# Kernel optimization log

Measured on AMD Instinct MI355X. Metric: run time of the kernel, lower is better.

## Reference

```python
import jax, jax.numpy as jnp
import numpy as np
from math import pi as PI

N_NODES = 50000
N_EDGES = 1000000
HIDDEN = 128
N_GAUSS = 50
N_FILT = 128
N_COLORS = 4
CUTOFF = 10.0
LOG2 = float(np.log(2.0))


def setup_inputs() -> dict:
    key = jax.random.key(0)
    ks = jax.random.split(key, 16)
    glorot = jax.nn.initializers.glorot_uniform()
    inp = {
        "x": jax.random.normal(ks[0], (N_NODES, HIDDEN), jnp.float32),
        "edge_index": jax.random.randint(ks[1], (2, N_EDGES), 0, N_NODES),
        "edge_weight": jax.random.uniform(ks[2], (N_EDGES,), jnp.float32) * CUTOFF,
        "edge_attr": jax.random.normal(ks[3], (N_EDGES, N_GAUSS), jnp.float32),
        "colors": jax.random.randint(ks[4], (N_EDGES,), 0, N_COLORS),
        # ColoredMLP params, stacked over colors
        "mlp1_w": glorot(ks[5], (N_COLORS, N_FILT, N_GAUSS), jnp.float32),
        "mlp1_b": jnp.zeros((N_COLORS, N_FILT), jnp.float32),
        "mlp2_w": glorot(ks[6], (N_COLORS, N_FILT, N_FILT), jnp.float32),
        "mlp2_b": jnp.zeros((N_COLORS, N_FILT), jnp.float32),
        # CFConv linears
        "lin1_w": glorot(ks[7], (N_FILT, HIDDEN), jnp.float32),
        "lin2_w": glorot(ks[8], (HIDDEN, N_FILT), jnp.float32),
        "lin2_b": jnp.zeros((HIDDEN,), jnp.float32),
        # final Linear
        "lin_w": glorot(ks[9], (HIDDEN, HIDDEN), jnp.float32),
        "lin_b": jnp.zeros((HIDDEN,), jnp.float32),
    }
    return inp


def shifted_softplus(v):
    return jax.nn.softplus(v) - LOG2


def colored_mlp(edge_attr, colors, mlp1_w, mlp1_b, mlp2_w, mlp2_b):
    # per-color small MLP; loop over the small fixed color set, select by mask
    out = jnp.zeros((edge_attr.shape[0], N_FILT), edge_attr.dtype)
    for c in range(N_COLORS):
        h = shifted_softplus(edge_attr @ mlp1_w[c].T + mlp1_b[c])
        h = h @ mlp2_w[c].T + mlp2_b[c]
        out = jnp.where((colors == c)[:, None], h, out)
    return out


def reference(x, edge_index, edge_weight, edge_attr, colors,
              mlp1_w, mlp1_b, mlp2_w, mlp2_b,
              lin1_w, lin2_w, lin2_b, lin_w, lin_b):
    # cosine cutoff
    C = 0.5 * (jnp.cos(edge_weight * PI / CUTOFF) + 1.0)  # [E]
    W = colored_mlp(edge_attr, colors, mlp1_w, mlp1_b, mlp2_w, mlp2_b) * C[:, None]  # [E,F]
    h = x @ lin1_w.T  # [N,F]
    src, dst = edge_index[0], edge_index[1]
    msg = h[src] * W  # gather + modulate, [E,F]
    agg = jax.ops.segment_sum(msg, dst, num_segments=N_NODES)  # scatter-add, [N,F]
    out = agg @ lin2_w.T + lin2_b  # [N,H]
    out = shifted_softplus(out)
    out = out @ lin_w.T + lin_b
    return out
```

## Files before the change

### kernel.cpp

```cpp
#include <hip/hip_runtime.h>
#include <math.h>

#define N_NODES_ 50000
#define N_EDGES_ 1000000
#define HID 128
#define NG 50
#define NF 128
#define NCOL 4
#define CSEG 258048
#define NKEY (NCOL * N_NODES_)
#define CHUNK 625
#define NCHUNK_PER_C 80
#define NCHUNK (NCOL * NCHUNK_PER_C)

typedef short s16x8 __attribute__((ext_vector_type(8)));
typedef float f32x4 __attribute__((ext_vector_type(4)));

__device__ __forceinline__ float sspf(float v) {
    float r = __logf(1.f + __expf(v)) - 0.69314718055994531f;
    return (v > 15.f) ? (v - 0.69314718055994531f) : r;
}

__device__ __forceinline__ unsigned int f2b(float f) {
    unsigned int u = __float_as_uint(f);
    return (u + 0x7fffu + ((u >> 16) & 1u)) >> 16;
}

__global__ __launch_bounds__(256) void hist_kernel(const int* __restrict__ colors,
                                                   const int* __restrict__ edge_index,
                                                   int* __restrict__ hist) {
    int e = blockIdx.x * 256 + threadIdx.x;
    if (e < N_EDGES_) {
        int key = colors[e] * N_NODES_ + edge_index[N_EDGES_ + e];
        atomicAdd(&hist[key], 1);
    }
}

__global__ __launch_bounds__(256) void scan1_kernel(int* __restrict__ hist,
                                                    int* __restrict__ csum) {
    __shared__ int s[CHUNK];
    int b = blockIdx.x;
    int c = b / NCHUNK_PER_C, ch = b % NCHUNK_PER_C;
    int gofs = c * N_NODES_ + ch * CHUNK;
    for (int i = threadIdx.x; i < CHUNK; i += 256) s[i] = hist[gofs + i];
    __syncthreads();
    if (threadIdx.x == 0) {
        int run = 0;
        for (int i = 0; i < CHUNK; ++i) { int t = s[i]; s[i] = run; run += t; }
        csum[b] = run;
    }
    __syncthreads();
    for (int i = threadIdx.x; i < CHUNK; i += 256) hist[gofs + i] = s[i];
}

__global__ __launch_bounds__(64) void scan2_kernel(const int* __restrict__ csum,
                                                   int* __restrict__ cbase,
                                                   int* __restrict__ g_cnt) {
    int c = threadIdx.x;
    if (c < NCOL) {
        int run = 0;
        for (int j = 0; j < NCHUNK_PER_C; ++j) {
            cbase[c * NCHUNK_PER_C + j] = run;
            run += csum[c * NCHUNK_PER_C + j];
        }
        g_cnt[c] = run;
    }
}

__global__ __launch_bounds__(256) void scan3_kernel(int* __restrict__ hist,
                                                    const int* __restrict__ cbase) {
    int b = blockIdx.x;
    int c = b / NCHUNK_PER_C, ch = b % NCHUNK_PER_C;
    int gofs = c * N_NODES_ + ch * CHUNK;
    int add = cbase[b];
    for (int i = threadIdx.x; i < CHUNK; i += 256) hist[gofs + i] += add;
}

__global__ __launch_bounds__(256) void scatter_kernel(const int* __restrict__ colors,
                                                      const int* __restrict__ edge_index,
                                                      int* __restrict__ base,
                                                      int* __restrict__ eid_s) {
    int e = blockIdx.x * 256 + threadIdx.x;
    if (e < N_EDGES_) {
        int c = colors[e];
        int key = c * N_NODES_ + edge_index[N_EDGES_ + e];
        int r = atomicAdd(&base[key], 1);
        eid_s[c * CSEG + r] = e;
    }
}

__global__ __launch_bounds__(256) void wconv_kernel(const float* __restrict__ m1w,
                                                    const float* __restrict__ m2w,
                                                    unsigned short* __restrict__ m1b16,
                                                    unsigned short* __restrict__ m2b16) {
    int idx = blockIdx.x * 256 + threadIdx.x;
    if (idx < NCOL * NF * 64) {
        int c = idx / (NF * 64);
        int rem = idx % (NF * 64);
        int n = rem / 64, k = rem % 64;
        float v = (k < NG) ? m1w[(c * NF + n) * NG + k] : 0.f;
        m1b16[idx] = (unsigned short)f2b(v);
    } else if (idx < NCOL * NF * 64 + NCOL * NF * NF) {
        int j = idx - NCOL * NF * 64;
        m2b16[j] = (unsigned short)f2b(m2w[j]);
    }
}

__global__ __launch_bounds__(256, 4) void passA_kernel(
    const int* __restrict__ edge_index, const float* __restrict__ edge_weight,
    const float* __restrict__ edge_attr,
    const unsigned short* __restrict__ m1b16, const unsigned short* __restrict__ m2b16,
    const float* __restrict__ m1bias, const float* __restrict__ m2bias,
    const float* __restrict__ h, const int* __restrict__ eid_s,
    const int* __restrict__ g_cnt, float* __restrict__ agg) {

    __shared__ __align__(16) unsigned short eaT[64][80];
    __shared__ __align__(16) unsigned short tsT[64][144];

    int c = blockIdx.x >> 12;
    int tile = blockIdx.x & 4095;
    int cnt = g_cnt[c];
    if (tile * 64 >= cnt) return;
    int pos0 = c * CSEG + tile * 64;

    int tid = threadIdx.x;
    int wv = tid >> 6;
    int l15 = tid & 15;
    int q = (tid >> 4) & 3;
    int e = (wv << 4) | l15;

    int eid = eid_s[pos0 + e];
    int sidx = 0, d = -1;
    float cw = 0.f;
    if (eid >= 0) {
        sidx = edge_index[eid];
        d = edge_index[N_EDGES_ + eid];
        float ww = edge_weight[eid];
        cw = 0.5f * (__cosf(ww * 0.31415926535897932f) + 1.f);
    }

    {
        int r = tid >> 2, j0 = tid & 3;
        int eid2 = eid_s[pos0 + r];
        if (eid2 < 0) eid2 = 0;
        const float* ear = edge_attr + (size_t)eid2 * NG;
#pragma unroll
        for (int j = 0; j < 10; ++j) {
            int i2 = j0 + 4 * j;
            unsigned int pk = 0;
            if (i2 < 25) {
                float2 v = *(const float2*)(ear + 2 * i2);
                pk = f2b(v.x) | (f2b(v.y) << 16);
            }
            *(unsigned int*)&eaT[r][2 * i2] = pk;
        }
    }

    f32x4 acc[8];
#pragma unroll
    for (int m = 0; m < 8; ++m) acc[m] = (f32x4)(0.f);
    {
        const unsigned short* m1p = m1b16 + (size_t)c * NF * 64;
#pragma unroll
        for (int ks = 0; ks < 2; ++ks) {
            s16x8 bfrag = *(const s16x8*)&eaT[e][q * 8 + 32 * ks];
#pragma unroll
            for (int m = 0; m < 8; ++m) {
                s16x8 afrag = *(const s16x8*)(m1p + (m * 16 + l15) * 64 + q * 8 + 32 * ks);
                acc[m] = __builtin_amdgcn_mfma_f32_16x16x32_bf16(afrag, bfrag, acc[m], 0, 0, 0);
            }
        }
    }
    {
        const float* b1p = m1bias + c * NF;
#pragma unroll
        for (int m = 0; m < 8; ++m) {
            int n0 = m * 16 + q * 4;
            f32x4 bv = *(const f32x4*)(b1p + n0);
            float t0 = sspf(acc[m][0] + bv[0]);
            float t1 = sspf(acc[m][1] + bv[1]);
            float t2 = sspf(acc[m][2] + bv[2]);
            float t3 = sspf(acc[m][3] + bv[3]);
            unsigned int p0 = f2b(t0) | (f2b(t1) << 16);
            unsigned int p1 = f2b(t2) | (f2b(t3) << 16);
            uint2 pk; pk.x = p0; pk.y = p1;
            *(uint2*)&tsT[e][n0] = pk;
        }
    }

    f32x4 acc2[8];
#pragma unroll
    for (int m = 0; m < 8; ++m) acc2[m] = (f32x4)(0.f);
    {
        const unsigned short* m2p = m2b16 + (size_t)c * NF * NF;
#pragma unroll
        for (int ks = 0; ks < 4; ++ks) {
            s16x8 bfrag = *(const s16x8*)&tsT[e][q * 8 + 32 * ks];
#pragma unroll
            for (int m = 0; m < 8; ++m) {
                s16x8 afrag = *(const s16x8*)(m2p + (m * 16 + l15) * NF + q * 8 + 32 * ks);
                acc2[m] = __builtin_amdgcn_mfma_f32_16x16x32_bf16(afrag, bfrag, acc2[m], 0, 0, 0);
            }
        }
    }

    {
        const float* hrow = h + (size_t)sidx * HID;
        const float* b2p = m2bias + c * NF;
#pragma unroll
        for (int m = 0; m < 8; ++m) {
            int n0 = m * 16 + q * 4;
            f32x4 hv = *(const f32x4*)(hrow + n0);
            f32x4 bv = *(const f32x4*)(b2p + n0);
            acc2[m][0] = (acc2[m][0] + bv[0]) * cw * hv[0];
            acc2[m][1] = (acc2[m][1] + bv[1]) * cw * hv[1];
            acc2[m][2] = (acc2[m][2] + bv[2]) * cw * hv[2];
            acc2[m][3] = (acc2[m][3] + bv[3]) * cw * hv[3];
        }
    }

    int dprev = __shfl_up(d, 1, 16);
#pragma unroll
    for (int dd = 1; dd < 16; dd <<= 1) {
        int dn = __shfl_down(d, dd, 16);
        bool same = (dn == d) && (l15 + dd < 16);
#pragma unroll
        for (int m = 0; m < 8; ++m) {
#pragma unroll
            for (int j = 0; j < 4; ++j) {
                float vn = __shfl_down(acc2[m][j], dd, 16);
                if (same) acc2[m][j] += vn;
            }
        }
    }

    bool head = (d >= 0) && (l15 == 0 || d != dprev);
    if (head) {
        float* ap = agg + (size_t)d * HID + (q << 2);
#pragma unroll
        for (int m = 0; m < 8; ++m) {
            atomicAdd(ap + m * 16 + 0, acc2[m][0]);
            atomicAdd(ap + m * 16 + 1, acc2[m][1]);
            atomicAdd(ap + m * 16 + 2, acc2[m][2]);
            atomicAdd(ap + m * 16 + 3, acc2[m][3]);
        }
    }
}

__device__ __forceinline__ void fma_2x8(float (&acc)[2][8], float2 a, float4 b0, float4 b1) {
    acc[0][0] += a.x * b0.x; acc[0][1] += a.x * b0.y;
    acc[0][2] += a.x * b0.z; acc[0][3] += a.x * b0.w;
    acc[0][4] += a.x * b1.x; acc[0][5] += a.x * b1.y;
    acc[0][6] += a.x * b1.z; acc[0][7] += a.x * b1.w;
    acc[1][0] += a.y * b0.x; acc[1][1] += a.y * b0.y;
    acc[1][2] += a.y * b0.z; acc[1][3] += a.y * b0.w;
    acc[1][4] += a.y * b1.x; acc[1][5] += a.y * b1.y;
    acc[1][6] += a.y * b1.z; acc[1][7] += a.y * b1.w;
}

__device__ __forceinline__ void load_wT32(const float4* __restrict__ w4, int kc,
                                          float (*wT)[132], int tid) {
#pragma unroll
    for (int i = 0; i < 4; ++i) {
        int lin = tid + 256 * i;
        int col = lin >> 3;
        int m = lin & 7;
        float4 v = w4[col * 32 + (kc >> 2) + m];
        wT[4 * m + 0][col] = v.x;
        wT[4 * m + 1][col] = v.y;
        wT[4 * m + 2][col] = v.z;
        wT[4 * m + 3][col] = v.w;
    }
}

__global__ __launch_bounds__(256) void lin1_kernel(const float* __restrict__ x,
                                                   const float* __restrict__ w,
                                                   float* __restrict__ h) {
    __shared__ float xT[HID][36];
    __shared__ float wT[32][132];
    int tid = threadIdx.x;
    int tx = tid & 15, ty = tid >> 4;
    int r0 = blockIdx.x * 32;
    const float4* x4 = (const float4*)x;
#pragma unroll
    for (int i = 0; i < 4; ++i) {
        int lin = tid + 256 * i;
        int r = lin >> 5, m = lin & 31;
        int rr = r0 + r; if (rr > N_NODES_ - 1) rr = N_NODES_ - 1;
        float4 v = x4[rr * 32 + m];
        xT[4 * m + 0][r] = v.x; xT[4 * m + 1][r] = v.y;
        xT[4 * m + 2][r] = v.z; xT[4 * m + 3][r] = v.w;
    }
    float acc[2][8] = {};
    for (int kc = 0; kc < HID; kc += 32) {
        __syncthreads();
        load_wT32((const float4*)w, kc, wT, tid);
        __syncthreads();
#pragma unroll 8
        for (int k2 = 0; k2 < 32; ++k2) {
            float2 a = *(const float2*)&xT[kc + k2][2 * ty];
            float4 b0 = *(const float4*)&wT[k2][8 * tx];
            float4 b1 = *(const float4*)&wT[k2][8 * tx + 4];
            fma_2x8(acc, a, b0, b1);
        }
    }
    float4* h4 = (float4*)h;
#pragma unroll
    for (int i = 0; i < 2; ++i) {
        int row = r0 + 2 * ty + i;
        if (row < N_NODES_) {
            h4[row * 32 + 2 * tx]     = make_float4(acc[i][0], acc[i][1], acc[i][2], acc[i][3]);
            h4[row * 32 + 2 * tx + 1] = make_float4(acc[i][4], acc[i][5], acc[i][6], acc[i][7]);
        }
    }
}

__global__ __launch_bounds__(256) void out_kernel(
    const float* __restrict__ agg,
    const float* __restrict__ w2, const float* __restrict__ b2,
    const float* __restrict__ w3, const float* __restrict__ b3,
    float* __restrict__ out) {
    __shared__ float sT[HID][36];
    __shared__ float wT[32][132];
    int tid = threadIdx.x;
    int tx = tid & 15, ty = tid >> 4;
    int r0 = blockIdx.x * 32;
    const float4* a4 = (const float4*)agg;
#pragma unroll
    for (int i = 0; i < 4; ++i) {
        int lin = tid + 256 * i;
        int r = lin >> 5, m = lin & 31;
        int rr = r0 + r; if (rr > N_NODES_ - 1) rr = N_NODES_ - 1;
        float4 v = a4[rr * 32 + m];
        sT[4 * m + 0][r] = v.x; sT[4 * m + 1][r] = v.y;
        sT[4 * m + 2][r] = v.z; sT[4 * m + 3][r] = v.w;
    }
    float acc[2][8] = {};
    for (int kc = 0; kc < HID; kc += 32) {
        __syncthreads();
        load_wT32((const float4*)w2, kc, wT, tid);
        __syncthreads();
#pragma unroll 8
        for (int k2 = 0; k2 < 32; ++k2) {
            float2 a = *(const float2*)&sT[kc + k2][2 * ty];
            float4 c0 = *(const float4*)&wT[k2][8 * tx];
            float4 c1 = *(const float4*)&wT[k2][8 * tx + 4];
            fma_2x8(acc, a, c0, c1);
        }
    }
    __syncthreads();
#pragma unroll
    for (int j = 0; j < 8; ++j) {
        int col = 8 * tx + j;
        float bbv = b2[col];
        sT[col][2 * ty]     = sspf(acc[0][j] + bbv);
        sT[col][2 * ty + 1] = sspf(acc[1][j] + bbv);
    }
    float acc2[2][8] = {};
    for (int kc = 0; kc < HID; kc += 32) {
        __syncthreads();
        load_wT32((const float4*)w3, kc, wT, tid);
        __syncthreads();
#pragma unroll 8
        for (int k2 = 0; k2 < 32; ++k2) {
            float2 a = *(const float2*)&sT[kc + k2][2 * ty];
            float4 c0 = *(const float4*)&wT[k2][8 * tx];
            float4 c1 = *(const float4*)&wT[k2][8 * tx + 4];
            fma_2x8(acc2, a, c0, c1);
        }
    }
    float4* out4 = (float4*)out;
#pragma unroll
    for (int i = 0; i < 2; ++i) {
        int row = r0 + 2 * ty + i;
        if (row < N_NODES_) {
            out4[row * 32 + 2 * tx] = make_float4(
                acc2[i][0] + b3[8 * tx + 0], acc2[i][1] + b3[8 * tx + 1],
                acc2[i][2] + b3[8 * tx + 2], acc2[i][3] + b3[8 * tx + 3]);
            out4[row * 32 + 2 * tx + 1] = make_float4(
                acc2[i][4] + b3[8 * tx + 4], acc2[i][5] + b3[8 * tx + 5],
                acc2[i][6] + b3[8 * tx + 6], acc2[i][7] + b3[8 * tx + 7]);
        }
    }
}

extern "C" void kernel_launch(void* const* d_in, const int* in_sizes, int n_in,
                              void* d_out, int out_size, void* d_ws, size_t ws_size,
                              hipStream_t stream) {
    const float* x           = (const float*)d_in[0];
    const int*   edge_index  = (const int*)d_in[1];
    const float* edge_weight = (const float*)d_in[2];
    const float* edge_attr   = (const float*)d_in[3];
    const int*   colors      = (const int*)d_in[4];
    const float* m1w         = (const float*)d_in[5];
    const float* m1b         = (const float*)d_in[6];
    const float* m2w         = (const float*)d_in[7];
    const float* m2b         = (const float*)d_in[8];
    const float* lin1w       = (const float*)d_in[9];
    const float* lin2w       = (const float*)d_in[10];
    const float* lin2b       = (const float*)d_in[11];
    const float* linw        = (const float*)d_in[12];
    const float* linb        = (const float*)d_in[13];
    float* out = (float*)d_out;

    char* ws = (char*)d_ws;
    float* h      = (float*)(ws);
    float* agg    = (float*)(ws + 25600000);
    int*   eid_s  = (int*)(ws + 51200000);
    int*   base   = (int*)(ws + 55328768);
    int*   csum   = (int*)(ws + 56128768);
    int*   cbase  = (int*)(ws + 56130048);
    int*   g_cnt  = (int*)(ws + 56131328);
    unsigned short* m1b16 = (unsigned short*)(ws + 56131392);
    unsigned short* m2b16 = (unsigned short*)(ws + 56196928);

    hipMemsetAsync(agg, 0, (size_t)N_NODES_ * HID * sizeof(float), stream);
    hipMemsetAsync(base, 0, NKEY * sizeof(int), stream);
    hipMemsetAsync(eid_s, 0xFF, (size_t)NCOL * CSEG * sizeof(int), stream);

    hist_kernel<<<(N_EDGES_ + 255) / 256, 256, 0, stream>>>(colors, edge_index, base);
    scan1_kernel<<<NCHUNK, 256, 0, stream>>>(base, csum);
    scan2_kernel<<<1, 64, 0, stream>>>(csum, cbase, g_cnt);
    scan3_kernel<<<NCHUNK, 256, 0, stream>>>(base, cbase);
    scatter_kernel<<<(N_EDGES_ + 255) / 256, 256, 0, stream>>>(colors, edge_index, base, eid_s);
    wconv_kernel<<<(NCOL * NF * 64 + NCOL * NF * NF + 255) / 256, 256, 0, stream>>>(m1w, m2w, m1b16, m2b16);
    lin1_kernel<<<(N_NODES_ + 31) / 32, 256, 0, stream>>>(x, lin1w, h);
    passA_kernel<<<NCOL * 4096, 256, 0, stream>>>(edge_index, edge_weight, edge_attr,
                                                  m1b16, m2b16, m1b, m2b, h, eid_s, g_cnt, agg);
    out_kernel<<<(N_NODES_ + 31) / 32, 256, 0, stream>>>(agg, lin2w, lin2b, linw, linb, out);
}
```

Measured before the change: 1.097 ms.

## Load edge_attr MFMA fragments directly into registers, swizzle tsT LDS, raise occupancy

Drops the eaT shared-memory staging for edge attributes. Each lane now loads its own B-fragment for the first MLP layer straight from global memory and converts it to bf16 in registers. The tsT buffer gets an XOR swizzle on its byte addresses to cut LDS bank conflicts on the uint2 writes and 16-byte reads. Launch bounds rise from 4 to 8 waves per SIMD to allow more occupancy. The trade-offs are less coalesced global loads for edge_attr and possible register spills under the tighter register budget.

```diff
diff --git a/kernel.cpp b/kernel.cpp
--- a/kernel.cpp
+++ b/kernel.cpp
@@ -106,7 +106,7 @@
     }
 }
 
-__global__ __launch_bounds__(256, 4) void passA_kernel(
+__global__ __launch_bounds__(256, 8) void passA_kernel(
     const int* __restrict__ edge_index, const float* __restrict__ edge_weight,
     const float* __restrict__ edge_attr,
     const unsigned short* __restrict__ m1b16, const unsigned short* __restrict__ m2b16,
@@ -114,8 +114,9 @@
     const float* __restrict__ h, const int* __restrict__ eid_s,
     const int* __restrict__ g_cnt, float* __restrict__ agg) {
 
-    __shared__ __align__(16) unsigned short eaT[64][80];
     __shared__ __align__(16) unsigned short tsT[64][144];
+#define TS_BYTE(e_, col2_) ((((e_) * 288 + (col2_)) ^ (((e_) & 7) << 4)))
+    char* tsb = (char*)&tsT[0][0];
 
     int c = blockIdx.x >> 12;
     int tile = blockIdx.x & 4095;
@@ -139,21 +140,31 @@
         cw = 0.5f * (__cosf(ww * 0.31415926535897932f) + 1.f);
     }
 
+    union { s16x8 v; unsigned int u[4]; } bf0, bf1;
     {
-        int r = tid >> 2, j0 = tid & 3;
-        int eid2 = eid_s[pos0 + r];
-        if (eid2 < 0) eid2 = 0;
-        const float* ear = edge_attr + (size_t)eid2 * NG;
-#pragma unroll
-        for (int j = 0; j < 10; ++j) {
-            int i2 = j0 + 4 * j;
-            unsigned int pk = 0;
-            if (i2 < 25) {
-                float2 v = *(const float2*)(ear + 2 * i2);
-                pk = f2b(v.x) | (f2b(v.y) << 16);
-            }
-            *(unsigned int*)&eaT[r][2 * i2] = pk;
-        }
+        const float* ear = edge_attr + (size_t)((eid >= 0) ? eid : 0) * NG;
+        float2 a0 = *(const float2*)(ear + q * 8 + 0);
+        float2 a1 = *(const float2*)(ear + q * 8 + 2);
+        float2 a2 = *(const float2*)(ear + q * 8 + 4);
+        float2 a3 = *(const float2*)(ear + q * 8 + 6);
+        bf0.u[0] = f2b(a0.x) | (f2b(a0.y) << 16);
+        bf0.u[1] = f2b(a1.x) | (f2b(a1.y) << 16);
+        bf0.u[2] = f2b(a2.x) | (f2b(a2.y) << 16);
+        bf0.u[3] = f2b(a3.x) | (f2b(a3.y) << 16);
+        float2 c0 = make_float2(0.f, 0.f), c1 = c0, c2 = c0, c3 = c0;
+        int k1 = 32 + q * 8;
+        if (q < 2) {
+            c0 = *(const float2*)(ear + k1 + 0);
+            c1 = *(const float2*)(ear + k1 + 2);
+            c2 = *(const float2*)(ear + k1 + 4);
+            c3 = *(const float2*)(ear + k1 + 6);
+        } else if (q == 2) {
+            c0 = *(const float2*)(ear + 48);
+        }
+        bf1.u[0] = f2b(c0.x) | (f2b(c0.y) << 16);
+        bf1.u[1] = f2b(c1.x) | (f2b(c1.y) << 16);
+        bf1.u[2] = f2b(c2.x) | (f2b(c2.y) << 16);
+        bf1.u[3] = f2b(c3.x) | (f2b(c3.y) << 16);
     }
 
     f32x4 acc[8];
@@ -162,13 +173,14 @@
     {
         const unsigned short* m1p = m1b16 + (size_t)c * NF * 64;
 #pragma unroll
-        for (int ks = 0; ks < 2; ++ks) {
-            s16x8 bfrag = *(const s16x8*)&eaT[e][q * 8 + 32 * ks];
-#pragma unroll
-            for (int m = 0; m < 8; ++m) {
-                s16x8 afrag = *(const s16x8*)(m1p + (m * 16 + l15) * 64 + q * 8 + 32 * ks);
-                acc[m] = __builtin_amdgcn_mfma_f32_16x16x32_bf16(afrag, bfrag, acc[m], 0, 0, 0);
-            }
+        for (int m = 0; m < 8; ++m) {
+            s16x8 afrag0 = *(const s16x8*)(m1p + (m * 16 + l15) * 64 + q * 8);
+            acc[m] = __builtin_amdgcn_mfma_f32_16x16x32_bf16(afrag0, bf0.v, acc[m], 0, 0, 0);
+        }
+#pragma unroll
+        for (int m = 0; m < 8; ++m) {
+            s16x8 afrag1 = *(const s16x8*)(m1p + (m * 16 + l15) * 64 + q * 8 + 32);
+            acc[m] = __builtin_amdgcn_mfma_f32_16x16x32_bf16(afrag1, bf1.v, acc[m], 0, 0, 0);
         }
     }
     {
@@ -184,7 +196,7 @@
             unsigned int p0 = f2b(t0) | (f2b(t1) << 16);
             unsigned int p1 = f2b(t2) | (f2b(t3) << 16);
             uint2 pk; pk.x = p0; pk.y = p1;
-            *(uint2*)&tsT[e][n0] = pk;
+            *(uint2*)(tsb + TS_BYTE(e, n0 * 2)) = pk;
         }
     }
 
@@ -195,7 +207,7 @@
         const unsigned short* m2p = m2b16 + (size_t)c * NF * NF;
 #pragma unroll
         for (int ks = 0; ks < 4; ++ks) {
-            s16x8 bfrag = *(const s16x8*)&tsT[e][q * 8 + 32 * ks];
+            s16x8 bfrag = *(const s16x8*)(tsb + TS_BYTE(e, (q * 8 + 32 * ks) * 2));
 #pragma unroll
             for (int m = 0; m < 8; ++m) {
                 s16x8 afrag = *(const s16x8*)(m2p + (m * 16 + l15) * NF + q * 8 + 32 * ks);
@@ -245,6 +257,7 @@
             atomicAdd(ap + m * 16 + 3, acc2[m][3]);
         }
     }
+#undef TS_BYTE
 }
 
 __device__ __forceinline__ void fma_2x8(float (&acc)[2][8], float2 a, float4 b0, float4 b1) {
```

New measurement: 1.798 ms. 64.0% more time.
